# Kernel tuning notes

Hardware: AMD Instinct MI355X
Metric: run time of the kernel (lower is better)

## Reference

```python
import jax, jax.numpy as jnp
import numpy as np

# Static sizes (match input_specs / init_kwargs)
N = 10000       # nodes
E = 160000      # edges
L = 2           # num_layers
S = 256         # scalar_dim (hidden_dim)
V = 32          # vec_dim (1o and 1e channel count)
L2 = 16         # 2e channel count
NRBF = 16
TDIM = 128
ESD = NRBF + 16 + 20 + 8 + S + S + TDIM   # 700 edge-scalar dim
WOUT = S + 4 * V + L2                     # 400 per-edge TP path weights
ADA = 2 * S + 2 * V + L2                  # 592 AdaLN modulation dim
FEAT = S + 3 * V + 3 * V + 5 * L2         # 528 flattened irreps width
DEG_INV = 1.0 / np.sqrt(E / N)            # 1/sqrt(avg degree) message normalizer


def setup_inputs() -> dict:
    key = jax.random.key(0)
    ks = jax.random.split(key, 30)
    f32 = jnp.float32

    def nrm(k, shape, scale=1.0):
        return jax.random.normal(k, shape, dtype=f32) * scale

    inp = {
        "h": nrm(ks[0], (N, FEAT)),
        "coords": nrm(ks[1], (N, 3), 3.0),
        "edge_ref_dist": jax.random.uniform(ks[2], (E,), dtype=f32) * 4.0,
        "t_emb": nrm(ks[3], (N, TDIM)),
        # per-layer learned params, stacked on leading L axis
        "etype_emb": nrm(ks[4], (L, 9, 16), 0.5),
        "btype_emb": nrm(ks[5], (L, 6, 8), 0.5),
        "bconj_emb": nrm(ks[6], (L, 3, 4), 0.5),
        "bring_emb": nrm(ks[7], (L, 3, 4), 0.5),
        "bstereo_emb": nrm(ks[8], (L, 5, 4), 0.5),
        "ref_W": nrm(ks[9], (L, 3, 8), 1.0 / np.sqrt(3)),
        "ref_b": jnp.zeros((L, 8), f32),
        "edge_W": nrm(ks[10], (L, ESD, WOUT), 1.0 / np.sqrt(ESD)),
        "edge_b": jnp.zeros((L, WOUT), f32),
        "sv_W": nrm(ks[11], (L, S, V), 1.0 / np.sqrt(S)),
        "proj_s": nrm(ks[12], (L, S, S), 1.0 / np.sqrt(S)),
        "proj_v1": nrm(ks[13], (L, V, V), 1.0 / np.sqrt(V)),
        "proj_v2": nrm(ks[14], (L, V, V), 1.0 / np.sqrt(V)),
        "proj_l2": nrm(ks[15], (L, L2, L2), 1.0 / np.sqrt(L2)),
        "ada_W": nrm(ks[16], (L, TDIM, ADA), 1.0 / np.sqrt(TDIM)),
        "ada_b": jnp.zeros((L, ADA), f32),
        # int graph structure
        "edge_index": jax.random.randint(ks[17], (2, E), 0, N),
        "edge_type": jax.random.randint(ks[18], (E,), 0, 9),
        "edge_bond_type": jax.random.randint(ks[19], (E,), 0, 6),
        "edge_bond_conjugated": jax.random.randint(ks[20], (E,), 0, 3),
        "edge_bond_in_ring": jax.random.randint(ks[21], (E,), 0, 3),
        "edge_bond_stereo": jax.random.randint(ks[22], (E,), 0, 5),
    }
    return inp


def _forward(h, coords, edge_ref_dist, t_emb,
             etype_emb, btype_emb, bconj_emb, bring_emb, bstereo_emb,
             ref_W, ref_b, edge_W, edge_b, sv_W,
             proj_s, proj_v1, proj_v2, proj_l2, ada_W, ada_b,
             edge_index, edge_type, edge_bond_type,
             edge_bond_conjugated, edge_bond_in_ring, edge_bond_stereo):
    src, dst = edge_index[0], edge_index[1]
    # geometry (shared across layers)
    diff = coords[dst] - coords[src]                    # [E,3]
    dist = jnp.linalg.norm(diff, axis=-1)               # [E]
    centers = jnp.linspace(0.0, 10.0, NRBF)
    width = 10.0 / NRBF
    rbf = jnp.exp(-(((dist[:, None] - centers) / width) ** 2))   # [E,NRBF]
    Y1 = diff / (dist[:, None] + 1e-8)                  # unit direction, l=1 SH
    has_ref = (edge_ref_dist > 0).astype(jnp.float32)
    delta = dist - edge_ref_dist
    ref_feat = jnp.stack([jnp.abs(delta), delta, has_ref], axis=-1)  # [E,3]

    for l in range(L):
        # split irreps blocks
        s = h[:, :S]
        v1o = h[:, S:S + 3 * V].reshape(N, V, 3)
        v1e = h[:, S + 3 * V:S + 6 * V].reshape(N, V, 3)
        q2e = h[:, S + 6 * V:].reshape(N, L2, 5)

        # edge scalar features (embeddings + RBF + node scalars + time)
        e_type = etype_emb[l][edge_type]
        e_bond = jnp.concatenate([
            btype_emb[l][edge_bond_type], bconj_emb[l][edge_bond_conjugated],
            bring_emb[l][edge_bond_in_ring], bstereo_emb[l][edge_bond_stereo]], axis=-1)
        e_ref = ref_feat @ ref_W[l] + ref_b[l]
        edge_scalars = jnp.concatenate(
            [rbf, e_type, e_bond, e_ref, s[src], s[dst], t_emb[dst]], axis=-1)  # [E,700]

        # per-edge tensor-product path weights
        w = edge_scalars @ edge_W[l] + edge_b[l]          # [E,400]
        w_s, w_v1, w_sv, w_v2, w_cx, w_l2 = jnp.split(
            w, [S, S + V, S + 2 * V, S + 3 * V, S + 4 * V], axis=-1)

        sv = s @ sv_W[l]                                  # [N,V] scalar->vec gate channels
        # equivariant messages
        m_s = w_s * s[src]                                                   # 0e x 0e -> 0e
        m_v1o = w_v1[:, :, None] * v1o[src] \
              + (w_sv * sv[src])[:, :, None] * Y1[:, None, :]                # 0e x 1o -> 1o
        m_v1e = w_v2[:, :, None] * v1e[src] \
              + w_cx[:, :, None] * jnp.cross(v1o[src], Y1[:, None, :])       # 1o x 1o -> 1e
        m_l2 = w_l2[:, :, None] * q2e[src]                                   # 0e x 2e -> 2e

        # scatter-sum to destination nodes
        agg_s = jax.ops.segment_sum(m_s, dst, num_segments=N) * DEG_INV
        agg_v1o = jax.ops.segment_sum(m_v1o, dst, num_segments=N) * DEG_INV
        agg_v1e = jax.ops.segment_sum(m_v1e, dst, num_segments=N) * DEG_INV
        agg_l2 = jax.ops.segment_sum(m_l2, dst, num_segments=N) * DEG_INV

        # per-irrep channel-mixing projection, scalar activation
        u_s = jax.nn.silu(agg_s @ proj_s[l])
        u_v1o = jnp.einsum('nci,cd->ndi', agg_v1o, proj_v1[l])
        u_v1e = jnp.einsum('nci,cd->ndi', agg_v1e, proj_v2[l])
        u_l2 = jnp.einsum('nci,cd->ndi', agg_l2, proj_l2[l])

        # residual
        s = s + u_s
        v1o = v1o + u_v1o
        v1e = v1e + u_v1e
        q2e = q2e + u_l2

        # equivariant AdaLN conditioned on t_emb
        ada = t_emb @ ada_W[l] + ada_b[l]
        sc, sh_, g1, g2, gl = jnp.split(ada, [S, 2 * S, 2 * S + V, 2 * S + 2 * V], axis=-1)
        mu = s.mean(axis=-1, keepdims=True)
        var = s.var(axis=-1, keepdims=True)
        s = (s - mu) / jnp.sqrt(var + 1e-5) * (1.0 + sc) + sh_

        def vnorm(v, g):
            rms = jnp.sqrt(jnp.mean(jnp.sum(v * v, axis=-1), axis=-1, keepdims=True) + 1e-5)
            return v / rms[:, :, None] * (1.0 + g)[:, :, None]

        v1o = vnorm(v1o, g1)
        v1e = vnorm(v1e, g2)
        q2e = vnorm(q2e, gl)

        h = jnp.concatenate(
            [s, v1o.reshape(N, 3 * V), v1e.reshape(N, 3 * V), q2e.reshape(N, 5 * L2)], axis=-1)
    return h


def reference(h, coords, edge_ref_dist, t_emb,
              etype_emb, btype_emb, bconj_emb, bring_emb, bstereo_emb,
              ref_W, ref_b, edge_W, edge_b, sv_W,
              proj_s, proj_v1, proj_v2, proj_l2, ada_W, ada_b,
              edge_index, edge_type, edge_bond_type,
              edge_bond_conjugated, edge_bond_in_ring, edge_bond_stereo):
    return _forward(h, coords, edge_ref_dist, t_emb,
                    etype_emb, btype_emb, bconj_emb, bring_emb, bstereo_emb,
                    ref_W, ref_b, edge_W, edge_b, sv_W,
                    proj_s, proj_v1, proj_v2, proj_l2, ada_W, ada_b,
                    edge_index, edge_type, edge_bond_type,
                    edge_bond_conjugated, edge_bond_in_ring, edge_bond_stereo)
```

## Files before the change

kernel.cpp:

```cpp
#include <hip/hip_runtime.h>
#include <math.h>

#define NN 10000
#define NE 160000
#define SDIM 256
#define VDIM 32
#define L2DIM 16
#define TDIM 128
#define FEAT 528
#define WOUT 400
#define ADA 592
#define DEG_INV 0.25f

#define ETM 16
#define WLP 404
#define AP1 72
#define AP2 392
#define AP3 264
#define HSP 536

typedef short bf16x8 __attribute__((ext_vector_type(8)));
typedef float f32x4 __attribute__((ext_vector_type(4)));

__device__ __forceinline__ unsigned short f2bf(float f) {
    unsigned int u = __float_as_uint(f);
    u += 0x7fffu + ((u >> 16) & 1u);
    return (unsigned short)(u >> 16);
}
__device__ __forceinline__ float bf2f(unsigned short b) {
    return __uint_as_float(((unsigned int)b) << 16);
}

__global__ __launch_bounds__(256) void hist_kernel(const int* __restrict__ eidx,
                                                   int* __restrict__ cnt) {
    int e = blockIdx.x * 256 + threadIdx.x;
    if (e < NE) atomicAdd(&cnt[eidx[NE + e]], 1);
}

__global__ __launch_bounds__(1024) void scan_kernel(const int* __restrict__ cnt,
                                                    int* __restrict__ cursor) {
    __shared__ int sc[1024];
    int tid = threadIdx.x;
    int base = tid * 10;
    int loc[10];
    int s = 0;
    if (base < NN) {
        #pragma unroll
        for (int j = 0; j < 10; ++j) { loc[j] = cnt[base + j]; s += loc[j]; }
    }
    sc[tid] = s;
    __syncthreads();
    for (int off = 1; off < 1024; off <<= 1) {
        int v = sc[tid];
        int add = (tid >= off) ? sc[tid - off] : 0;
        __syncthreads();
        sc[tid] = v + add;
        __syncthreads();
    }
    int run = sc[tid] - s;
    if (base < NN) {
        #pragma unroll
        for (int j = 0; j < 10; ++j) { cursor[base + j] = run; run += loc[j]; }
    }
}

__global__ __launch_bounds__(256) void scatter_kernel(const int* __restrict__ eidx,
                                                      int* __restrict__ cursor,
                                                      int* __restrict__ perm) {
    int e = blockIdx.x * 256 + threadIdx.x;
    if (e < NE) {
        int d = eidx[NE + e];
        int p = atomicAdd(&cursor[d], 1);
        perm[p] = e;
    }
}

#define O1 25600
#define O2 332800
#define O3 408576
#define O4 416768
#define O5 482304
__global__ __launch_bounds__(256) void prep_kernel(
    const float* __restrict__ W, const float* __restrict__ adaW,
    const float* __restrict__ svW, const float* __restrict__ projs,
    unsigned short* __restrict__ Wt1, unsigned short* __restrict__ Bn,
    unsigned short* __restrict__ Ba, unsigned short* __restrict__ Bsv,
    unsigned short* __restrict__ Ps)
{
    int idx = blockIdx.x * 256 + threadIdx.x;
    if (idx < O1) {
        int c = idx >> 6, k = idx & 63;
        float v = (k < 60) ? W[(size_t)k * WOUT + c] : 0.f;
        Wt1[idx] = f2bf(v);
    } else if (idx < O2) {
        int i = idx - O1;
        int c = i / 384, k = i - c * 384;
        float v;
        if (c < WOUT) v = (k < 256) ? W[(size_t)(60 + k) * WOUT + c] : 0.f;
        else {
            int c2 = c - WOUT;
            v = (k < 256) ? W[(size_t)(316 + k) * WOUT + c2]
                          : W[(size_t)(572 + (k - 256)) * WOUT + c2];
        }
        Bn[i] = f2bf(v);
    } else if (idx < O3) {
        int i = idx - O2;
        int c = i >> 7, k = i & 127;
        Ba[i] = f2bf(adaW[(size_t)k * ADA + c]);
    } else if (idx < O4) {
        int i = idx - O3;
        int c = i >> 8, k = i & 255;
        Bsv[i] = f2bf(svW[(size_t)k * VDIM + c]);
    } else if (idx < O5) {
        int i = idx - O4;
        int c = i >> 8, k = i & 255;
        Ps[i] = f2bf(projs[(size_t)k * SDIM + c]);
    }
}

struct us4 { unsigned short x, y, z, w; };
__global__ __launch_bounds__(256) void hb_kernel(const float* __restrict__ h,
                                                 unsigned short* __restrict__ hb) {
    int i = blockIdx.x * 256 + threadIdx.x;
    if (i >= NN * FEAT / 4) return;
    float4 v = ((const float4*)h)[i];
    us4 o;
    o.x = f2bf(v.x); o.y = f2bf(v.y); o.z = f2bf(v.z); o.w = f2bf(v.w);
    ((us4*)hb)[i] = o;
}

__global__ __launch_bounds__(256) void nodeproj_kernel(
    const unsigned short* __restrict__ hb, const float* __restrict__ t_emb,
    const unsigned short* __restrict__ Bn, const unsigned short* __restrict__ Ba,
    const unsigned short* __restrict__ Bsv,
    const float* __restrict__ edge_b, const float* __restrict__ adab,
    unsigned short* __restrict__ srcdst, float* __restrict__ ada_out,
    float* __restrict__ sv)
{
    __shared__ unsigned short As2[32 * AP2];
    const int tid = threadIdx.x;
    const int n0 = blockIdx.x * 32;

    for (int e = 0; e < 32; ++e) {
        int n = n0 + e;
        As2[e * AP2 + tid] = (n < NN) ? hb[(size_t)n * FEAT + tid] : 0;
        if (tid < 128) {
            float v1 = (n < NN) ? t_emb[(size_t)n * TDIM + tid] : 0.f;
            As2[e * AP2 + 256 + tid] = f2bf(v1);
        }
    }
    __syncthreads();

    const int wid = tid >> 6, lane = tid & 63;
    const int lr = lane & 15, lkb = (lane >> 4) << 3;
    const int rbase = (lane >> 4) << 2;

    {
        const int nt0 = wid * 13;
        f32x4 acc[2][13];
        #pragma unroll
        for (int m = 0; m < 2; ++m)
            #pragma unroll
            for (int t = 0; t < 13; ++t) acc[m][t] = (f32x4){0.f, 0.f, 0.f, 0.f};

        for (int ks = 0; ks < 12; ++ks) {
            int kb = ks * 32 + lkb;
            bf16x8 a0 = *(const bf16x8*)&As2[lr * AP2 + kb];
            bf16x8 a1 = *(const bf16x8*)&As2[(16 + lr) * AP2 + kb];
            #pragma unroll
            for (int t = 0; t < 13; ++t) {
                int tile = nt0 + t;
                if (tile < 50) {
                    bf16x8 b = *(const bf16x8*)&Bn[(size_t)(tile * 16 + lr) * 384 + kb];
                    acc[0][t] = __builtin_amdgcn_mfma_f32_16x16x32_bf16(a0, b, acc[0][t], 0, 0, 0);
                    acc[1][t] = __builtin_amdgcn_mfma_f32_16x16x32_bf16(a1, b, acc[1][t], 0, 0, 0);
                }
            }
        }
        #pragma unroll
        for (int t = 0; t < 13; ++t) {
            int tile = nt0 + t;
            if (tile < 50) {
                int col = tile * 16 + lr;
                float badd = (col >= WOUT) ? edge_b[col - WOUT] : 0.f;
                #pragma unroll
                for (int m = 0; m < 2; ++m) {
                    #pragma unroll
                    for (int r = 0; r < 4; ++r) {
                        int n = n0 + m * 16 + rbase + r;
                        if (n < NN) srcdst[(size_t)n * 800 + col] = f2bf(acc[m][t][r] + badd);
                    }
                }
            }
        }
    }

    {
        const int nt0a = wid * 9;
        f32x4 acc2[2][10];
        #pragma unroll
        for (int m = 0; m < 2; ++m)
            #pragma unroll
            for (int t = 0; t < 10; ++t) acc2[m][t] = (f32x4){0.f, 0.f, 0.f, 0.f};

        for (int ks = 0; ks < 4; ++ks) {
            int kin = ks * 32 + lkb;
            bf16x8 a0 = *(const bf16x8*)&As2[lr * AP2 + 256 + kin];
            bf16x8 a1 = *(const bf16x8*)&As2[(16 + lr) * AP2 + 256 + kin];
            #pragma unroll
            for (int t = 0; t < 10; ++t) {
                int tile = nt0a + t;
                if (tile < 37) {
                    bf16x8 b = *(const bf16x8*)&Ba[(size_t)(tile * 16 + lr) * 128 + kin];
                    acc2[0][t] = __builtin_amdgcn_mfma_f32_16x16x32_bf16(a0, b, acc2[0][t], 0, 0, 0);
                    acc2[1][t] = __builtin_amdgcn_mfma_f32_16x16x32_bf16(a1, b, acc2[1][t], 0, 0, 0);
                }
            }
        }
        #pragma unroll
        for (int t = 0; t < 10; ++t) {
            int tile = nt0a + t;
            if (tile < 37) {
                int col = tile * 16 + lr;
                float badd = adab[col];
                #pragma unroll
                for (int m = 0; m < 2; ++m) {
                    #pragma unroll
                    for (int r = 0; r < 4; ++r) {
                        int n = n0 + m * 16 + rbase + r;
                        if (n < NN) ada_out[(size_t)n * ADA + col] = acc2[m][t][r] + badd;
                    }
                }
            }
        }
    }

    if (wid < 2) {
        f32x4 accs[2];
        accs[0] = (f32x4){0.f, 0.f, 0.f, 0.f};
        accs[1] = (f32x4){0.f, 0.f, 0.f, 0.f};
        for (int ks = 0; ks < 8; ++ks) {
            int kb = ks * 32 + lkb;
            bf16x8 a0 = *(const bf16x8*)&As2[lr * AP2 + kb];
            bf16x8 a1 = *(const bf16x8*)&As2[(16 + lr) * AP2 + kb];
            bf16x8 b = *(const bf16x8*)&Bsv[(size_t)(wid * 16 + lr) * 256 + kb];
            accs[0] = __builtin_amdgcn_mfma_f32_16x16x32_bf16(a0, b, accs[0], 0, 0, 0);
            accs[1] = __builtin_amdgcn_mfma_f32_16x16x32_bf16(a1, b, accs[1], 0, 0, 0);
        }
        int col = wid * 16 + lr;
        #pragma unroll
        for (int m = 0; m < 2; ++m) {
            #pragma unroll
            for (int r = 0; r < 4; ++r) {
                int n = n0 + m * 16 + rbase + r;
                if (n < NN) sv[(size_t)n * VDIM + col] = accs[m][r];
            }
        }
    }
}

__global__ __launch_bounds__(256) void edge_kernel(
    const unsigned short* __restrict__ hb, const float* __restrict__ coords,
    const float* __restrict__ erd, const float* __restrict__ sv,
    const unsigned short* __restrict__ Wt1, const unsigned short* __restrict__ srcdst,
    const int* __restrict__ perm, const int* __restrict__ eidx,
    const int* __restrict__ etype, const int* __restrict__ ebt,
    const int* __restrict__ ebc, const int* __restrict__ ebr,
    const int* __restrict__ ebs,
    const float* __restrict__ etype_emb, const float* __restrict__ btype_emb,
    const float* __restrict__ bconj_emb, const float* __restrict__ bring_emb,
    const float* __restrict__ bstereo_emb,
    const float* __restrict__ refW, const float* __restrict__ refb,
    float* __restrict__ agg)
{
    __shared__ unsigned short wl[ETM * WLP];
    __shared__ unsigned short hsl[ETM * HSP];
    __shared__ float svl[ETM * VDIM];
    __shared__ unsigned short As[ETM * AP1];
    __shared__ int srcl[ETM], dstl[ETM];
    __shared__ int itype[ETM], ibt[ETM], ibc[ETM], ibr[ETM], ibs[ETM];
    __shared__ float distl[ETM], erdl[ETM], y1l[ETM][3];

    const int tid = threadIdx.x;
    const int e0 = blockIdx.x * ETM;

    if (tid < ETM) {
        int ge = perm[e0 + tid];
        int s = eidx[ge], d = eidx[NE + ge];
        srcl[tid] = s; dstl[tid] = d;
        itype[tid] = etype[ge]; ibt[tid] = ebt[ge]; ibc[tid] = ebc[ge];
        ibr[tid] = ebr[ge]; ibs[tid] = ebs[ge];
        float dx = coords[d*3+0] - coords[s*3+0];
        float dy = coords[d*3+1] - coords[s*3+1];
        float dz = coords[d*3+2] - coords[s*3+2];
        float dist = sqrtf(dx*dx + dy*dy + dz*dz);
        distl[tid] = dist;
        float inv = 1.f / (dist + 1e-8f);
        y1l[tid][0] = dx * inv; y1l[tid][1] = dy * inv; y1l[tid][2] = dz * inv;
        erdl[tid] = erd[ge];
    }
    __syncthreads();

    {
        for (int i = tid; i < ETM * 66; i += 256) {
            int e = i / 66, j = i - e * 66;
            bf16x8 v = *(const bf16x8*)&hb[(size_t)srcl[e] * FEAT + j * 8];
            *(bf16x8*)&hsl[e * HSP + j * 8] = v;
        }
        for (int i = tid; i < ETM * VDIM; i += 256) {
            int e = i >> 5, c = i & 31;
            svl[i] = sv[(size_t)srcl[e] * VDIM + c];
        }
    }

    {
        const int k = tid & 63;
        const int ebase = tid >> 6;
        #pragma unroll
        for (int it = 0; it < 4; ++it) {
            int e = it * 4 + ebase;
            float de = distl[e];
            float v;
            if (k >= 60) v = 0.f;
            else if (k < 16) { float x = (de - (float)k * (10.f/15.f)) * 1.6f; v = expf(-x*x); }
            else if (k < 32) v = etype_emb[itype[e]*16 + (k-16)];
            else if (k < 40) v = btype_emb[ibt[e]*8 + (k-32)];
            else if (k < 44) v = bconj_emb[ibc[e]*4 + (k-40)];
            else if (k < 48) v = bring_emb[ibr[e]*4 + (k-44)];
            else if (k < 52) v = bstereo_emb[ibs[e]*4 + (k-48)];
            else {
                int j = k - 52;
                float dd = de - erdl[e];
                float hr = erdl[e] > 0.f ? 1.f : 0.f;
                v = fabsf(dd)*refW[j] + dd*refW[8+j] + hr*refW[16+j] + refb[j];
            }
            As[e * AP1 + k] = f2bf(v);
        }
    }
    __syncthreads();

    const int wid = tid >> 6, lane = tid & 63;
    const int lr = lane & 15, lkb = (lane >> 4) << 3;
    const int nt0 = wid * 6;
    {
        f32x4 acc[7];
        #pragma unroll
        for (int t = 0; t < 7; ++t) acc[t] = (f32x4){0.f, 0.f, 0.f, 0.f};

        #pragma unroll
        for (int ks = 0; ks < 2; ++ks) {
            int kb = ks * 32 + lkb;
            bf16x8 a0 = *(const bf16x8*)&As[lr * AP1 + kb];
            #pragma unroll
            for (int t = 0; t < 7; ++t) {
                bf16x8 b = *(const bf16x8*)&Wt1[(size_t)((nt0 + t) * 16 + lr) * 64 + kb];
                acc[t] = __builtin_amdgcn_mfma_f32_16x16x32_bf16(a0, b, acc[t], 0, 0, 0);
            }
        }
        const int rbase = (lane >> 4) << 2;
        int se[4], de_[4];
        #pragma unroll
        for (int r = 0; r < 4; ++r) { se[r] = srcl[rbase + r]; de_[r] = dstl[rbase + r]; }
        #pragma unroll
        for (int t = 0; t < 7; ++t) {
            const int col = (nt0 + t) * 16 + lr;
            #pragma unroll
            for (int r = 0; r < 4; ++r) {
                float add = bf2f(srcdst[(size_t)se[r] * 800 + col])
                          + bf2f(srcdst[(size_t)de_[r] * 800 + 400 + col]);
                wl[(rbase + r) * WLP + col] = f2bf(acc[t][r] + add);
            }
        }
    }
    __syncthreads();

    {
        int cls = 0, cc = 0, ii = 0, ia = 0, ib = 0, hoff = 0, wB1 = 0, wB2 = 0;
        if (tid < 96)       { cls = 0; cc = tid / 3;        ii = tid % 3;        hoff = 256 + tid; wB1 = 256 + cc; wB2 = 288 + cc; }
        else if (tid < 192) { int j = tid - 96; cls = 1; cc = j / 3; ii = j % 3; hoff = 352 + j;   wB1 = 320 + cc; wB2 = 352 + cc; }
        else                { int j = tid - 192; cls = 2; cc = j / 5;            hoff = 448 + j;   wB1 = 384 + cc; }
        ia = (ii + 1) % 3; ib = (ii + 2) % 3;

        const bool hasC = tid < 16;
        const int jC = 64 + tid;
        const int hoffC = 448 + jC;
        const int wC = 384 + jC / 5;

        float accA = 0.f, accB = 0.f, accC = 0.f;
        for (int e = 0; e < ETM; ++e) {
            const unsigned short* hs = &hsl[e * HSP];
            accA = fmaf(bf2f(wl[e * WLP + tid]), bf2f(hs[tid]), accA);
            float m;
            if (cls == 0) {
                float wv1 = bf2f(wl[e * WLP + wB1]), wsv = bf2f(wl[e * WLP + wB2]);
                m = wv1 * bf2f(hs[hoff]) + wsv * svl[e * VDIM + cc] * y1l[e][ii];
            } else if (cls == 1) {
                float wv2 = bf2f(wl[e * WLP + wB1]), wcx = bf2f(wl[e * WLP + wB2]);
                float va = bf2f(hs[256 + cc * 3 + ia]), vb = bf2f(hs[256 + cc * 3 + ib]);
                m = wv2 * bf2f(hs[hoff]) + wcx * (va * y1l[e][ib] - vb * y1l[e][ia]);
            } else {
                m = bf2f(wl[e * WLP + wB1]) * bf2f(hs[hoff]);
            }
            accB += m;
            if (hasC) accC = fmaf(bf2f(wl[e * WLP + wC]), bf2f(hs[hoffC]), accC);

            bool fl = (e == ETM - 1) || (dstl[e + 1] != dstl[e]);
            if (fl) {
                int d = dstl[e];
                atomicAdd(&agg[(size_t)d * FEAT + tid], accA);
                atomicAdd(&agg[(size_t)d * FEAT + 256 + tid], accB);
                if (hasC) atomicAdd(&agg[(size_t)d * FEAT + hoffC], accC);
                accA = 0.f; accB = 0.f; accC = 0.f;
            }
        }
    }
}

__global__ __launch_bounds__(256) void proj_kernel(
    const float* __restrict__ agg, const unsigned short* __restrict__ Ps,
    float* __restrict__ us_buf)
{
    __shared__ unsigned short As3[32 * AP3];
    const int tid = threadIdx.x;
    const int n0 = blockIdx.x * 32;

    for (int e = 0; e < 32; ++e) {
        int n = n0 + e;
        float v = (n < NN) ? agg[(size_t)n * FEAT + tid] * DEG_INV : 0.f;
        As3[e * AP3 + tid] = f2bf(v);
    }
    __syncthreads();

    const int wid = tid >> 6, lane = tid & 63;
    const int lr = lane & 15, lkb = (lane >> 4) << 3;
    const int rbase = (lane >> 4) << 2;
    const int nt0 = wid * 4;

    f32x4 acc[2][4];
    #pragma unroll
    for (int m = 0; m < 2; ++m)
        #pragma unroll
        for (int t = 0; t < 4; ++t) acc[m][t] = (f32x4){0.f, 0.f, 0.f, 0.f};

    for (int ks = 0; ks < 8; ++ks) {
        int kb = ks * 32 + lkb;
        bf16x8 a0 = *(const bf16x8*)&As3[lr * AP3 + kb];
        bf16x8 a1 = *(const bf16x8*)&As3[(16 + lr) * AP3 + kb];
        #pragma unroll
        for (int t = 0; t < 4; ++t) {
            bf16x8 b = *(const bf16x8*)&Ps[(size_t)((nt0 + t) * 16 + lr) * 256 + kb];
            acc[0][t] = __builtin_amdgcn_mfma_f32_16x16x32_bf16(a0, b, acc[0][t], 0, 0, 0);
            acc[1][t] = __builtin_amdgcn_mfma_f32_16x16x32_bf16(a1, b, acc[1][t], 0, 0, 0);
        }
    }
    #pragma unroll
    for (int t = 0; t < 4; ++t) {
        int col = (nt0 + t) * 16 + lr;
        #pragma unroll
        for (int m = 0; m < 2; ++m) {
            #pragma unroll
            for (int r = 0; r < 4; ++r) {
                int n = n0 + m * 16 + rbase + r;
                if (n < NN) {
                    float x = acc[m][t][r];
                    us_buf[(size_t)n * SDIM + col] = x / (1.f + expf(-x));
                }
            }
        }
    }
}

__device__ __forceinline__ float block_reduce_sum(float v, float* red, int tid) {
    #pragma unroll
    for (int off = 32; off > 0; off >>= 1) v += __shfl_down(v, off, 64);
    if ((tid & 63) == 0) red[tid >> 6] = v;
    __syncthreads();
    float s = red[0] + red[1] + red[2] + red[3];
    __syncthreads();
    return s;
}

__global__ __launch_bounds__(256) void node_kernel(
    const float* __restrict__ hcur, const float* __restrict__ ada_buf,
    const float* __restrict__ agg, const float* __restrict__ us_buf,
    const float* __restrict__ proj_v1, const float* __restrict__ proj_v2,
    const float* __restrict__ proj_l2,
    float* __restrict__ hnext, unsigned short* __restrict__ hbnext)
{
    const int n = blockIdx.x;
    const int tid = threadIdx.x;
    __shared__ float ada[ADA];
    __shared__ float av[272];
    __shared__ float vbuf[272];
    __shared__ float red[8];

    for (int i = tid; i < 272; i += 256)
        av[i] = agg[(size_t)n * FEAT + 256 + i] * DEG_INV;
    for (int r = 0; r < 3; ++r) {
        int col = r * 256 + tid;
        if (col < ADA) ada[col] = ada_buf[(size_t)n * ADA + col];
    }
    __syncthreads();

    float sn = hcur[(size_t)n * FEAT + tid] + us_buf[(size_t)n * SDIM + tid];

    if (tid < 96) {
        int d = tid / 3, i = tid - d * 3;
        float a = 0.f;
        #pragma unroll
        for (int c = 0; c < VDIM; ++c) a = fmaf(av[c*3 + i], proj_v1[c * VDIM + d], a);
        vbuf[tid] = hcur[(size_t)n * FEAT + SDIM + tid] + a;
    } else if (tid < 192) {
        int t2 = tid - 96;
        int d = t2 / 3, i = t2 - d * 3;
        float a = 0.f;
        #pragma unroll
        for (int c = 0; c < VDIM; ++c) a = fmaf(av[96 + c*3 + i], proj_v2[c * VDIM + d], a);
        vbuf[tid] = hcur[(size_t)n * FEAT + SDIM + 3*VDIM + t2] + a;
    }
    if (tid < 80) {
        int d = tid / 5, i = tid - d * 5;
        float a = 0.f;
        #pragma unroll
        for (int c = 0; c < L2DIM; ++c) a = fmaf(av[192 + c*5 + i], proj_l2[c * L2DIM + d], a);
        vbuf[192 + tid] = hcur[(size_t)n * FEAT + SDIM + 6*VDIM + tid] + a;
    }
    __syncthreads();

    float ssum = block_reduce_sum(sn, red, tid);
    float ssq  = block_reduce_sum(sn * sn, red, tid);
    float mu = ssum * (1.f / SDIM);
    float var = ssq * (1.f / SDIM) - mu * mu;
    float rstd = rsqrtf(var + 1e-5f);
    {
        float o = (sn - mu) * rstd * (1.f + ada[tid]) + ada[SDIM + tid];
        hnext[(size_t)n * FEAT + tid] = o;
        if (hbnext) hbnext[(size_t)n * FEAT + tid] = f2bf(o);
    }

    float q1 = (tid < 96) ? vbuf[tid] * vbuf[tid] : 0.f;
    float S1 = block_reduce_sum(q1, red, tid);
    float q2 = (tid >= 96 && tid < 192) ? vbuf[tid] * vbuf[tid] : 0.f;
    float S2 = block_reduce_sum(q2, red, tid);
    float q3 = (tid < 80) ? vbuf[192 + tid] * vbuf[192 + tid] : 0.f;
    float S3 = block_reduce_sum(q3, red, tid);

    float r1 = rsqrtf(S1 * (1.f / VDIM) + 1e-5f);
    float r2 = rsqrtf(S2 * (1.f / VDIM) + 1e-5f);
    float r3 = rsqrtf(S3 * (1.f / L2DIM) + 1e-5f);

    if (tid < 96) {
        int d = tid / 3;
        float o = vbuf[tid] * r1 * (1.f + ada[2*SDIM + d]);
        hnext[(size_t)n * FEAT + SDIM + tid] = o;
        if (hbnext) hbnext[(size_t)n * FEAT + SDIM + tid] = f2bf(o);
    } else if (tid < 192) {
        int t2 = tid - 96;
        int d = t2 / 3;
        float o = vbuf[tid] * r2 * (1.f + ada[2*SDIM + VDIM + d]);
        hnext[(size_t)n * FEAT + SDIM + 3*VDIM + t2] = o;
        if (hbnext) hbnext[(size_t)n * FEAT + SDIM + 3*VDIM + t2] = f2bf(o);
    }
    if (tid < 80) {
        int d = tid / 5;
        float o = vbuf[192 + tid] * r3 * (1.f + ada[2*SDIM + 2*VDIM + d]);
        hnext[(size_t)n * FEAT + SDIM + 6*VDIM + tid] = o;
        if (hbnext) hbnext[(size_t)n * FEAT + SDIM + 6*VDIM + tid] = f2bf(o);
    }
}

extern "C" void kernel_launch(void* const* d_in, const int* in_sizes, int n_in,
                              void* d_out, int out_size, void* d_ws, size_t ws_size,
                              hipStream_t stream) {
    const float* h_in   = (const float*)d_in[0];
    const float* coords = (const float*)d_in[1];
    const float* erd    = (const float*)d_in[2];
    const float* t_emb  = (const float*)d_in[3];
    const float* etype_emb   = (const float*)d_in[4];
    const float* btype_emb   = (const float*)d_in[5];
    const float* bconj_emb   = (const float*)d_in[6];
    const float* bring_emb   = (const float*)d_in[7];
    const float* bstereo_emb = (const float*)d_in[8];
    const float* refW   = (const float*)d_in[9];
    const float* refb   = (const float*)d_in[10];
    const float* edgeW  = (const float*)d_in[11];
    const float* edgeb  = (const float*)d_in[12];
    const float* svW    = (const float*)d_in[13];
    const float* proj_s = (const float*)d_in[14];
    const float* proj_v1= (const float*)d_in[15];
    const float* proj_v2= (const float*)d_in[16];
    const float* proj_l2= (const float*)d_in[17];
    const float* adaW   = (const float*)d_in[18];
    const float* adab   = (const float*)d_in[19];
    const int* eidx     = (const int*)d_in[20];
    const int* etype    = (const int*)d_in[21];
    const int* ebt      = (const int*)d_in[22];
    const int* ebc      = (const int*)d_in[23];
    const int* ebr      = (const int*)d_in[24];
    const int* ebs      = (const int*)d_in[25];

    float* ws_f     = (float*)d_ws;
    float* sv       = ws_f;
    float* agg      = sv + (size_t)NN * VDIM;
    float* h1       = agg + (size_t)NN * FEAT;
    float* ada_buf  = h1 + (size_t)NN * FEAT;
    float* us_buf   = ada_buf + (size_t)NN * ADA;
    unsigned short* srcdst = (unsigned short*)(us_buf + (size_t)NN * SDIM);
    unsigned short* hb     = srcdst + (size_t)NN * 800;
    unsigned short* Wt1    = hb + (size_t)NN * FEAT;
    unsigned short* Bn     = Wt1 + (size_t)WOUT * 64;
    unsigned short* Ba     = Bn + (size_t)800 * 384;
    unsigned short* Bsv    = Ba + (size_t)ADA * 128;
    unsigned short* Ps     = Bsv + (size_t)VDIM * 256;
    int* cnt    = (int*)(Ps + (size_t)SDIM * 256);
    int* cursor = cnt + NN;
    int* perm   = cursor + NN;

    hipMemsetAsync(cnt, 0, NN * sizeof(int), stream);
    hist_kernel<<<(NE + 255) / 256, 256, 0, stream>>>(eidx, cnt);
    scan_kernel<<<1, 1024, 0, stream>>>(cnt, cursor);
    scatter_kernel<<<(NE + 255) / 256, 256, 0, stream>>>(eidx, cursor, perm);
    hb_kernel<<<(NN * FEAT / 4 + 255) / 256, 256, 0, stream>>>(h_in, hb);

    for (int l = 0; l < 2; ++l) {
        const float* hcur = (l == 0) ? h_in : h1;
        float* hnext      = (l == 0) ? h1 : (float*)d_out;
        const float* W    = edgeW + (size_t)l * 700 * WOUT;

        hipMemsetAsync(agg, 0, (size_t)NN * FEAT * sizeof(float), stream);
        prep_kernel<<<(O5 + 255) / 256, 256, 0, stream>>>(
            W, adaW + (size_t)l * TDIM * ADA, svW + (size_t)l * SDIM * VDIM,
            proj_s + (size_t)l * SDIM * SDIM, Wt1, Bn, Ba, Bsv, Ps);
        nodeproj_kernel<<<(NN + 31) / 32, 256, 0, stream>>>(
            hb, t_emb, Bn, Ba, Bsv, edgeb + l * WOUT, adab + l * ADA,
            srcdst, ada_buf, sv);
        edge_kernel<<<NE / ETM, 256, 0, stream>>>(
            hb, coords, erd, sv, Wt1, srcdst, perm,
            eidx, etype, ebt, ebc, ebr, ebs,
            etype_emb + l * 144, btype_emb + l * 48, bconj_emb + l * 12,
            bring_emb + l * 12, bstereo_emb + l * 20,
            refW + l * 24, refb + l * 8,
            agg);
        proj_kernel<<<(NN + 31) / 32, 256, 0, stream>>>(agg, Ps, us_buf);
        node_kernel<<<NN, 256, 0, stream>>>(
            hcur, ada_buf, agg, us_buf,
            proj_v1 + l * VDIM * VDIM, proj_v2 + l * VDIM * VDIM,
            proj_l2 + l * L2DIM * L2DIM,
            hnext, (l == 0) ? hb : (unsigned short*)nullptr);
    }
}
```

Before: 762.5 us.

## Factor dst weight term out of per-edge loop; bf16 us_buf; wave-per-node node kernel

The per-edge gather of the destination half of srcdst is removed. Because that term is constant within a run of edges sharing the same dst, it is applied once at flush time, scaled by running sums of the per-edge factors. This roughly halves random global gathers in the edge kernel, at the cost of extra accumulators, and the bf16 rounding of the summed weights changes. Separately, us_buf is stored as bf16, and node_kernel now processes four nodes per block with one wave each, using shuffle reductions instead of shared-memory block reductions and many syncthreads.

```diff
diff --git a/kernel.cpp b/kernel.cpp
--- a/kernel.cpp
+++ b/kernel.cpp
@@ -358,16 +358,15 @@
             }
         }
         const int rbase = (lane >> 4) << 2;
-        int se[4], de_[4];
-        #pragma unroll
-        for (int r = 0; r < 4; ++r) { se[r] = srcl[rbase + r]; de_[r] = dstl[rbase + r]; }
+        int se[4];
+        #pragma unroll
+        for (int r = 0; r < 4; ++r) se[r] = srcl[rbase + r];
         #pragma unroll
         for (int t = 0; t < 7; ++t) {
             const int col = (nt0 + t) * 16 + lr;
             #pragma unroll
             for (int r = 0; r < 4; ++r) {
-                float add = bf2f(srcdst[(size_t)se[r] * 800 + col])
-                          + bf2f(srcdst[(size_t)de_[r] * 800 + 400 + col]);
+                float add = bf2f(srcdst[(size_t)se[r] * 800 + col]);
                 wl[(rbase + r) * WLP + col] = f2bf(acc[t][r] + add);
             }
         }
@@ -386,31 +385,52 @@
         const int hoffC = 448 + jC;
         const int wC = 384 + jC / 5;
 
-        float accA = 0.f, accB = 0.f, accC = 0.f;
+        float accA = 0.f, accAs = 0.f;
+        float accB = 0.f, accB1 = 0.f, accB2 = 0.f;
+        float accC = 0.f, accC1 = 0.f;
         for (int e = 0; e < ETM; ++e) {
             const unsigned short* hs = &hsl[e * HSP];
-            accA = fmaf(bf2f(wl[e * WLP + tid]), bf2f(hs[tid]), accA);
+            float sA = bf2f(hs[tid]);
+            accA = fmaf(bf2f(wl[e * WLP + tid]), sA, accA);
+            accAs += sA;
             float m;
             if (cls == 0) {
                 float wv1 = bf2f(wl[e * WLP + wB1]), wsv = bf2f(wl[e * WLP + wB2]);
-                m = wv1 * bf2f(hs[hoff]) + wsv * svl[e * VDIM + cc] * y1l[e][ii];
+                float a = bf2f(hs[hoff]);
+                float svy = svl[e * VDIM + cc] * y1l[e][ii];
+                m = wv1 * a + wsv * svy;
+                accB1 += a; accB2 += svy;
             } else if (cls == 1) {
                 float wv2 = bf2f(wl[e * WLP + wB1]), wcx = bf2f(wl[e * WLP + wB2]);
+                float a = bf2f(hs[hoff]);
                 float va = bf2f(hs[256 + cc * 3 + ia]), vb = bf2f(hs[256 + cc * 3 + ib]);
-                m = wv2 * bf2f(hs[hoff]) + wcx * (va * y1l[e][ib] - vb * y1l[e][ia]);
+                float cr = va * y1l[e][ib] - vb * y1l[e][ia];
+                m = wv2 * a + wcx * cr;
+                accB1 += a; accB2 += cr;
             } else {
-                m = bf2f(wl[e * WLP + wB1]) * bf2f(hs[hoff]);
+                float a = bf2f(hs[hoff]);
+                m = bf2f(wl[e * WLP + wB1]) * a;
+                accB1 += a;
             }
             accB += m;
-            if (hasC) accC = fmaf(bf2f(wl[e * WLP + wC]), bf2f(hs[hoffC]), accC);
+            if (hasC) {
+                float aC = bf2f(hs[hoffC]);
+                accC = fmaf(bf2f(wl[e * WLP + wC]), aC, accC);
+                accC1 += aC;
+            }
 
             bool fl = (e == ETM - 1) || (dstl[e + 1] != dstl[e]);
             if (fl) {
                 int d = dstl[e];
-                atomicAdd(&agg[(size_t)d * FEAT + tid], accA);
-                atomicAdd(&agg[(size_t)d * FEAT + 256 + tid], accB);
-                if (hasC) atomicAdd(&agg[(size_t)d * FEAT + hoffC], accC);
-                accA = 0.f; accB = 0.f; accC = 0.f;
+                const unsigned short* wd = &srcdst[(size_t)d * 800 + 400];
+                atomicAdd(&agg[(size_t)d * FEAT + tid], accA + bf2f(wd[tid]) * accAs);
+                float bout;
+                if (cls == 2) bout = accB + bf2f(wd[wB1]) * accB1;
+                else          bout = accB + bf2f(wd[wB1]) * accB1 + bf2f(wd[wB2]) * accB2;
+                atomicAdd(&agg[(size_t)d * FEAT + 256 + tid], bout);
+                if (hasC) atomicAdd(&agg[(size_t)d * FEAT + hoffC], accC + bf2f(wd[wC]) * accC1);
+                accA = 0.f; accAs = 0.f; accB = 0.f; accB1 = 0.f; accB2 = 0.f;
+                accC = 0.f; accC1 = 0.f;
             }
         }
     }
@@ -418,7 +438,7 @@
 
 __global__ __launch_bounds__(256) void proj_kernel(
     const float* __restrict__ agg, const unsigned short* __restrict__ Ps,
-    float* __restrict__ us_buf)
+    unsigned short* __restrict__ us_buf)
 {
     __shared__ unsigned short As3[32 * AP3];
     const int tid = threadIdx.x;
@@ -463,109 +483,125 @@
                 int n = n0 + m * 16 + rbase + r;
                 if (n < NN) {
                     float x = acc[m][t][r];
-                    us_buf[(size_t)n * SDIM + col] = x / (1.f + expf(-x));
+                    us_buf[(size_t)n * SDIM + col] = f2bf(x / (1.f + expf(-x)));
                 }
             }
         }
     }
-}
-
-__device__ __forceinline__ float block_reduce_sum(float v, float* red, int tid) {
-    #pragma unroll
-    for (int off = 32; off > 0; off >>= 1) v += __shfl_down(v, off, 64);
-    if ((tid & 63) == 0) red[tid >> 6] = v;
-    __syncthreads();
-    float s = red[0] + red[1] + red[2] + red[3];
-    __syncthreads();
-    return s;
 }
 
 __global__ __launch_bounds__(256) void node_kernel(
     const float* __restrict__ hcur, const float* __restrict__ ada_buf,
-    const float* __restrict__ agg, const float* __restrict__ us_buf,
-    const float* __restrict__ proj_v1, const float* __restrict__ proj_v2,
-    const float* __restrict__ proj_l2,
+    const float* __restrict__ agg, const unsigned short* __restrict__ us_buf,
+    const float* __restrict__ pv1, const float* __restrict__ pv2,
+    const float* __restrict__ pl2,
     float* __restrict__ hnext, unsigned short* __restrict__ hbnext)
 {
-    const int n = blockIdx.x;
+    __shared__ float plv1[VDIM * VDIM];
+    __shared__ float plv2[VDIM * VDIM];
+    __shared__ float pll2[L2DIM * L2DIM];
+    __shared__ float avl[4][272];
+
     const int tid = threadIdx.x;
-    __shared__ float ada[ADA];
-    __shared__ float av[272];
-    __shared__ float vbuf[272];
-    __shared__ float red[8];
-
-    for (int i = tid; i < 272; i += 256)
-        av[i] = agg[(size_t)n * FEAT + 256 + i] * DEG_INV;
-    for (int r = 0; r < 3; ++r) {
-        int col = r * 256 + tid;
-        if (col < ADA) ada[col] = ada_buf[(size_t)n * ADA + col];
-    }
+    for (int i = tid; i < VDIM * VDIM; i += 256) { plv1[i] = pv1[i]; plv2[i] = pv2[i]; }
+    if (tid < L2DIM * L2DIM) pll2[tid] = pl2[tid];
+
+    const int w = tid >> 6, lane = tid & 63;
+    const int n = blockIdx.x * 4 + w;
+    const size_t nb = (size_t)n * FEAT;
+    const size_t na = (size_t)n * ADA;
+
+    for (int i = lane; i < 272; i += 64) avl[w][i] = agg[nb + 256 + i] * DEG_INV;
     __syncthreads();
 
-    float sn = hcur[(size_t)n * FEAT + tid] + us_buf[(size_t)n * SDIM + tid];
-
-    if (tid < 96) {
-        int d = tid / 3, i = tid - d * 3;
-        float a = 0.f;
-        #pragma unroll
-        for (int c = 0; c < VDIM; ++c) a = fmaf(av[c*3 + i], proj_v1[c * VDIM + d], a);
-        vbuf[tid] = hcur[(size_t)n * FEAT + SDIM + tid] + a;
-    } else if (tid < 192) {
-        int t2 = tid - 96;
-        int d = t2 / 3, i = t2 - d * 3;
-        float a = 0.f;
-        #pragma unroll
-        for (int c = 0; c < VDIM; ++c) a = fmaf(av[96 + c*3 + i], proj_v2[c * VDIM + d], a);
-        vbuf[tid] = hcur[(size_t)n * FEAT + SDIM + 3*VDIM + t2] + a;
-    }
-    if (tid < 80) {
-        int d = tid / 5, i = tid - d * 5;
-        float a = 0.f;
-        #pragma unroll
-        for (int c = 0; c < L2DIM; ++c) a = fmaf(av[192 + c*5 + i], proj_l2[c * L2DIM + d], a);
-        vbuf[192 + tid] = hcur[(size_t)n * FEAT + SDIM + 6*VDIM + tid] + a;
-    }
-    __syncthreads();
-
-    float ssum = block_reduce_sum(sn, red, tid);
-    float ssq  = block_reduce_sum(sn * sn, red, tid);
+    float snv[4];
+    float ssum = 0.f, ssq = 0.f;
+    #pragma unroll
+    for (int j = 0; j < 4; ++j) {
+        int c = lane + 64 * j;
+        float v = hcur[nb + c] + bf2f(us_buf[(size_t)n * SDIM + c]);
+        snv[j] = v; ssum += v; ssq += v * v;
+    }
+    #pragma unroll
+    for (int off = 32; off > 0; off >>= 1) {
+        ssum += __shfl_xor(ssum, off, 64);
+        ssq  += __shfl_xor(ssq, off, 64);
+    }
     float mu = ssum * (1.f / SDIM);
     float var = ssq * (1.f / SDIM) - mu * mu;
     float rstd = rsqrtf(var + 1e-5f);
-    {
-        float o = (sn - mu) * rstd * (1.f + ada[tid]) + ada[SDIM + tid];
-        hnext[(size_t)n * FEAT + tid] = o;
-        if (hbnext) hbnext[(size_t)n * FEAT + tid] = f2bf(o);
-    }
-
-    float q1 = (tid < 96) ? vbuf[tid] * vbuf[tid] : 0.f;
-    float S1 = block_reduce_sum(q1, red, tid);
-    float q2 = (tid >= 96 && tid < 192) ? vbuf[tid] * vbuf[tid] : 0.f;
-    float S2 = block_reduce_sum(q2, red, tid);
-    float q3 = (tid < 80) ? vbuf[192 + tid] * vbuf[192 + tid] : 0.f;
-    float S3 = block_reduce_sum(q3, red, tid);
-
+    #pragma unroll
+    for (int j = 0; j < 4; ++j) {
+        int c = lane + 64 * j;
+        float o = (snv[j] - mu) * rstd * (1.f + ada_buf[na + c]) + ada_buf[na + SDIM + c];
+        hnext[nb + c] = o;
+        if (hbnext) hbnext[nb + c] = f2bf(o);
+    }
+
+    float vb[5];
+    float S1 = 0.f, S2 = 0.f, S3 = 0.f;
+    #pragma unroll
+    for (int j = 0; j < 5; ++j) {
+        int c = (j < 4) ? (lane + 64 * j) : (256 + lane);
+        bool ok = (j < 4) || (lane < 16);
+        float val = 0.f;
+        if (ok) {
+            if (c < 96) {
+                int d = c / 3, i = c - 3 * d;
+                float a = 0.f;
+                #pragma unroll
+                for (int k = 0; k < VDIM; ++k) a = fmaf(avl[w][k*3 + i], plv1[k * VDIM + d], a);
+                val = hcur[nb + SDIM + c] + a;
+                S1 += val * val;
+            } else if (c < 192) {
+                int c2 = c - 96;
+                int d = c2 / 3, i = c2 - 3 * d;
+                float a = 0.f;
+                #pragma unroll
+                for (int k = 0; k < VDIM; ++k) a = fmaf(avl[w][96 + k*3 + i], plv2[k * VDIM + d], a);
+                val = hcur[nb + SDIM + c] + a;
+                S2 += val * val;
+            } else {
+                int c2 = c - 192;
+                int d = c2 / 5, i = c2 - 5 * d;
+                float a = 0.f;
+                #pragma unroll
+                for (int k = 0; k < L2DIM; ++k) a = fmaf(avl[w][192 + k*5 + i], pll2[k * L2DIM + d], a);
+                val = hcur[nb + SDIM + c] + a;
+                S3 += val * val;
+            }
+        }
+        vb[j] = val;
+    }
+    #pragma unroll
+    for (int off = 32; off > 0; off >>= 1) {
+        S1 += __shfl_xor(S1, off, 64);
+        S2 += __shfl_xor(S2, off, 64);
+        S3 += __shfl_xor(S3, off, 64);
+    }
     float r1 = rsqrtf(S1 * (1.f / VDIM) + 1e-5f);
     float r2 = rsqrtf(S2 * (1.f / VDIM) + 1e-5f);
     float r3 = rsqrtf(S3 * (1.f / L2DIM) + 1e-5f);
 
-    if (tid < 96) {
-        int d = tid / 3;
-        float o = vbuf[tid] * r1 * (1.f + ada[2*SDIM + d]);
-        hnext[(size_t)n * FEAT + SDIM + tid] = o;
-        if (hbnext) hbnext[(size_t)n * FEAT + SDIM + tid] = f2bf(o);
-    } else if (tid < 192) {
-        int t2 = tid - 96;
-        int d = t2 / 3;
-        float o = vbuf[tid] * r2 * (1.f + ada[2*SDIM + VDIM + d]);
-        hnext[(size_t)n * FEAT + SDIM + 3*VDIM + t2] = o;
-        if (hbnext) hbnext[(size_t)n * FEAT + SDIM + 3*VDIM + t2] = f2bf(o);
-    }
-    if (tid < 80) {
-        int d = tid / 5;
-        float o = vbuf[192 + tid] * r3 * (1.f + ada[2*SDIM + 2*VDIM + d]);
-        hnext[(size_t)n * FEAT + SDIM + 6*VDIM + tid] = o;
-        if (hbnext) hbnext[(size_t)n * FEAT + SDIM + 6*VDIM + tid] = f2bf(o);
+    #pragma unroll
+    for (int j = 0; j < 5; ++j) {
+        int c = (j < 4) ? (lane + 64 * j) : (256 + lane);
+        bool ok = (j < 4) || (lane < 16);
+        if (ok) {
+            float o;
+            if (c < 96) {
+                int d = c / 3;
+                o = vb[j] * r1 * (1.f + ada_buf[na + 2*SDIM + d]);
+            } else if (c < 192) {
+                int d = (c - 96) / 3;
+                o = vb[j] * r2 * (1.f + ada_buf[na + 2*SDIM + VDIM + d]);
+            } else {
+                int d = (c - 192) / 5;
+                o = vb[j] * r3 * (1.f + ada_buf[na + 2*SDIM + 2*VDIM + d]);
+            }
+            hnext[nb + SDIM + c] = o;
+            if (hbnext) hbnext[nb + SDIM + c] = f2bf(o);
+        }
     }
 }
 
@@ -604,8 +640,9 @@
     float* agg      = sv + (size_t)NN * VDIM;
     float* h1       = agg + (size_t)NN * FEAT;
     float* ada_buf  = h1 + (size_t)NN * FEAT;
-    float* us_buf   = ada_buf + (size_t)NN * ADA;
-    unsigned short* srcdst = (unsigned short*)(us_buf + (size_t)NN * SDIM);
+    float* us_f     = ada_buf + (size_t)NN * ADA;
+    unsigned short* us_buf = (unsigned short*)us_f;
+    unsigned short* srcdst = (unsigned short*)(us_f + (size_t)NN * SDIM);
     unsigned short* hb     = srcdst + (size_t)NN * 800;
     unsigned short* Wt1    = hb + (size_t)NN * FEAT;
     unsigned short* Bn     = Wt1 + (size_t)WOUT * 64;
@@ -642,7 +679,7 @@
             refW + l * 24, refb + l * 8,
             agg);
         proj_kernel<<<(NN + 31) / 32, 256, 0, stream>>>(agg, Ps, us_buf);
-        node_kernel<<<NN, 256, 0, stream>>>(
+        node_kernel<<<NN / 4, 256, 0, stream>>>(
             hcur, ada_buf, agg, us_buf,
             proj_v1 + l * VDIM * VDIM, proj_v2 + l * VDIM * VDIM,
             proj_l2 + l * L2DIM * L2DIM,
```

Result: no change. 774.6 us (+1.6%).
